# Kernel tuning notes

Measured on AMD Instinct MI355X. Metric: run time of the kernel, lower is better.

The kernel has to match this reference:

```python
import jax, jax.numpy as jnp
import numpy as np

B, T, C, K = 8, 2048, 1024, 128

def setup_inputs() -> dict:
    key = jax.random.key(0)
    k1, k2, k3, k4 = jax.random.split(key, 4)
    scale = 0.02
    return {
        "x": jax.random.normal(k1, (B, T, C), dtype=jnp.float32),
        "Wq": jax.random.normal(k2, (C, K), dtype=jnp.float32) * scale,
        "Wk": jax.random.normal(k3, (C, K), dtype=jnp.float32) * scale,
        "Wv": jax.random.normal(k4, (C, K), dtype=jnp.float32) * scale,
    }

def reference(x, Wq, Wk, Wv):
    # Single-head causal self-attention (ModulUwagi.forward)
    q = jnp.einsum('btc,ck->btk', x, Wq)  # [B,T,K]
    k = jnp.einsum('btc,ck->btk', x, Wk)
    v = jnp.einsum('btc,ck->btk', x, Wv)
    hd = q.shape[-1]
    wei = jnp.einsum('btk,bsk->bts', q, k) * (hd ** -0.5)  # [B,T,T]
    causal = jnp.tril(jnp.ones((x.shape[1], x.shape[1]), dtype=bool))
    wei = jnp.where(causal, wei, -jnp.inf)
    wei = jax.nn.softmax(wei, axis=-1)
    out = jnp.einsum('bts,bsk->btk', wei, v)  # [B,T,K]
    return out
```

## Files before the change

kernel.cpp:

```cpp
#include <hip/hip_runtime.h>
#include <cmath>

#define Bn 8
#define Tn 2048
#define Cn 1024
#define Kn 128

typedef __attribute__((ext_vector_type(8))) short short8;
typedef __attribute__((ext_vector_type(4))) float f32x4;
typedef unsigned short u16;
typedef unsigned int u32;

#define NEGINF (-__builtin_huge_valf())

__device__ __forceinline__ u16 f2b(float f) {
    u32 u = __float_as_uint(f);
    u32 r = (u + 0x7FFFu + ((u >> 16) & 1u)) >> 16;
    return (u16)r;
}
__device__ __forceinline__ float b2f(u16 v) {
    u32 u = ((u32)v) << 16;
    return __uint_as_float(u);
}

__device__ __forceinline__ void load_lds16(const u16* g, u16* l) {
    __builtin_amdgcn_global_load_lds(
        (const __attribute__((address_space(1))) u32*)(g),
        (__attribute__((address_space(3))) u32*)(l), 16, 0, 0);
}

__global__ __launch_bounds__(256)
void prep_kernel(const float* __restrict__ Wq, const float* __restrict__ Wk,
                 const float* __restrict__ Wv, u16* __restrict__ Wt)
{
    int id = blockIdx.x * 256 + threadIdx.x;
    int w   = id >> 15;
    int rem = id & 32767;
    int c   = rem >> 5;
    int n4  = (rem & 31) << 2;
    const float* W = (w == 0) ? Wq : (w == 1) ? Wk : Wv;
    float4 v = *(const float4*)(W + (size_t)c * Kn + n4);
    u16* dst = Wt + (size_t)w * Kn * Cn;
    dst[(size_t)(n4 + 0) * Cn + c] = f2b(v.x);
    dst[(size_t)(n4 + 1) * Cn + c] = f2b(v.y);
    dst[(size_t)(n4 + 2) * Cn + c] = f2b(v.z);
    dst[(size_t)(n4 + 3) * Cn + c] = f2b(v.w);
}

__global__ __launch_bounds__(256)
void proj_kernel(const float* __restrict__ x, const u16* __restrict__ Wt,
                 u16* __restrict__ qkv)
{
    const int bid = blockIdx.x;
    const int g8  = bid >> 3, xr = bid & 7;
    const int w   = g8 % 3;
    const int rt  = (g8 / 3) * 8 + xr;
    const u16* wtg = Wt + (size_t)w * Kn * Cn;
    u16* outp = qkv + (size_t)w * Bn * Tn * Kn;
    const int row0 = rt * 128;
    const int tid  = threadIdx.x;
    const int lane = tid & 63;
    const int wid  = tid >> 6;
    const int l15  = lane & 15, lh = lane >> 4;
    const int wm0 = (wid >> 1) * 64, wn0 = (wid & 1) * 64;

    __shared__ u16 xs[128][72];
    __shared__ u16 wt[128][72];

    f32x4 acc[4][4];
    #pragma unroll
    for (int i = 0; i < 4; ++i)
        #pragma unroll
        for (int j = 0; j < 4; ++j) acc[i][j] = (f32x4){0.f, 0.f, 0.f, 0.f};

    for (int kk = 0; kk < Cn; kk += 64) {
        __syncthreads();
        #pragma unroll
        for (int i = 0; i < 8; ++i) {
            int idx = tid + i * 256;
            int r = idx >> 4, c4 = (idx & 15) << 2;
            float4 xv = *(const float4*)(x + (size_t)(row0 + r) * Cn + kk + c4);
            ushort4 pk = { f2b(xv.x), f2b(xv.y), f2b(xv.z), f2b(xv.w) };
            *(ushort4*)&xs[r][c4] = pk;
        }
        #pragma unroll
        for (int i = 0; i < 4; ++i) {
            int idx = tid + i * 256;
            int n = idx >> 3, c8 = (idx & 7) << 3;
            uint4 wv = *(const uint4*)(wtg + (size_t)n * Cn + kk + c8);
            *(uint4*)&wt[n][c8] = wv;
        }
        __syncthreads();
        #pragma unroll
        for (int kc = 0; kc < 2; ++kc) {
            const int coff = kc * 32 + lh * 8;
            short8 af[4], bf[4];
            #pragma unroll
            for (int mg = 0; mg < 4; ++mg)
                af[mg] = *(const short8*)&xs[wm0 + mg * 16 + l15][coff];
            #pragma unroll
            for (int ng = 0; ng < 4; ++ng)
                bf[ng] = *(const short8*)&wt[wn0 + ng * 16 + l15][coff];
            #pragma unroll
            for (int mg = 0; mg < 4; ++mg)
                #pragma unroll
                for (int ng = 0; ng < 4; ++ng)
                    acc[mg][ng] = __builtin_amdgcn_mfma_f32_16x16x32_bf16(
                        af[mg], bf[ng], acc[mg][ng], 0, 0, 0);
        }
    }
    #pragma unroll
    for (int mg = 0; mg < 4; ++mg)
        #pragma unroll
        for (int ng = 0; ng < 4; ++ng)
            #pragma unroll
            for (int r = 0; r < 4; ++r) {
                int m = row0 + wm0 + mg * 16 + lh * 4 + r;
                int n = wn0 + ng * 16 + l15;
                outp[(size_t)m * Kn + n] = f2b(acc[mg][ng][r]);
            }
}

__device__ const int g_job_qi[32] = {0, 1,1, 2,2,2, 3,3,3,3, 4,4,4,4,
                                     5,5,5,5,5, 6,6,6,6,6,6, 7,7,7,7,7,7,7};
__device__ const int g_sup_b[32] = {0, 0,4, 0,4,8, 0,4,8,12, 0,5,10,15,
                                    0,4,9,14,19, 0,4,9,14,18,23, 0,4,9,13,18,22,27};
__device__ const int g_sup_e[32] = {4, 4,8, 4,8,12, 4,8,12,16, 5,10,15,20,
                                    4,9,14,19,24, 4,9,14,18,23,28, 4,9,13,18,22,27,32};

__global__ __launch_bounds__(512, 2)
void attn_kernel(const u16* __restrict__ qg_, const u16* __restrict__ kg_,
                 const u16* __restrict__ vg_, u16* __restrict__ pO,
                 float* __restrict__ pM, float* __restrict__ pL)
{
    const int b   = blockIdx.x;
    const int job = blockIdx.y;
    const int qi  = g_job_qi[job];
    const int sb  = g_sup_b[job], se = g_sup_e[job];

    const u16* qw = qg_ + (size_t)b * Tn * Kn;
    const u16* kw = kg_ + (size_t)b * Tn * Kn;
    const u16* vw = vg_ + (size_t)b * Tn * Kn;

    const int tid  = threadIdx.x;
    const int lane = tid & 63;
    const int wid  = tid >> 6;
    const int l15  = lane & 15, lh = lane >> 4;

    const int q0 = qi * 256 + wid * 32;
    const int qmax_w = q0 + 31;

    __shared__ u16 lds[32768];

    short8 qf[2][4];
    #pragma unroll
    for (int g = 0; g < 2; ++g)
        #pragma unroll
        for (int kc = 0; kc < 4; ++kc)
            qf[g][kc] = *(const short8*)(qw + (size_t)(q0 + g * 16 + l15) * Kn
                                         + kc * 32 + lh * 8);

    f32x4 acc[8][2];
    #pragma unroll
    for (int dt = 0; dt < 8; ++dt)
        #pragma unroll
        for (int g = 0; g < 2; ++g) acc[dt][g] = (f32x4){0.f, 0.f, 0.f, 0.f};
    float m_g[2] = {NEGINF, NEGINF}, l_g[2] = {0.f, 0.f};

    const float scale = 0.08838834764831843f;

    auto stageK = [&](int sup, int buf) {
        const u16* src = kw + (size_t)sup * 64 * Kn;
        u16* dst = lds + buf * 8192;
        #pragma unroll
        for (int i = 0; i < 2; ++i) {
            int u = wid * 128 + i * 64 + lane;
            int row = u >> 4;
            int c16 = (u & 15) ^ (row & 7);
            load_lds16(src + (size_t)row * Kn + c16 * 8,
                       dst + (size_t)(wid * 128 + i * 64) * 8);
        }
    };
    auto loadV = [&](int sup, uint4* vr) {
        const u16* src = vw + (size_t)sup * 64 * Kn;
        #pragma unroll
        for (int r = 0; r < 2; ++r) {
            int s  = tid & 63;
            int u8 = (tid >> 6) + 8 * r;
            vr[r] = *(const uint4*)(src + (size_t)s * Kn + u8 * 8);
        }
    };
    auto writeV = [&](int buf, const uint4* vr) {
        u16* dst = lds + 16384 + buf * 8192;
        #pragma unroll
        for (int r = 0; r < 2; ++r) {
            int s  = tid & 63;
            int u8 = (tid >> 6) + 8 * r;
            const u16* e = (const u16*)&vr[r];
            #pragma unroll
            for (int j = 0; j < 8; ++j) {
                int d = u8 * 8 + j;
                dst[d * 64 + (((s >> 3) ^ j) << 3) + (s & 7)] = e[j];
            }
        }
    };

    uint4 vreg[2];
    stageK(sb, 0);
    loadV(sb, vreg);
    writeV(0, vreg);

    for (int sup = sb; sup < se; ++sup) {
        const int cur = (sup - sb) & 1;
        __syncthreads();
        const bool have_next = (sup + 1 < se);
        if (have_next) {
            stageK(sup + 1, cur ^ 1);
            loadV(sup + 1, vreg);
        }
        if (sup * 64 <= qmax_w) {
            const u16* Kb = lds + cur * 8192;
            const u16* Vb = lds + 16384 + cur * 8192;
            f32x4 sf[4][2];
            #pragma unroll
            for (int mt = 0; mt < 4; ++mt)
                #pragma unroll
                for (int g = 0; g < 2; ++g) sf[mt][g] = (f32x4){0.f,0.f,0.f,0.f};
            #pragma unroll
            for (int kc = 0; kc < 4; ++kc) {
                short8 a[4];
                #pragma unroll
                for (int mt = 0; mt < 4; ++mt) {
                    int row = mt * 16 + l15;
                    int ch  = (kc * 4 + lh) ^ (row & 7);
                    a[mt] = *(const short8*)(Kb + row * 128 + ch * 8);
                }
                #pragma unroll
                for (int mt = 0; mt < 4; ++mt)
                    #pragma unroll
                    for (int g = 0; g < 2; ++g)
                        sf[mt][g] = __builtin_amdgcn_mfma_f32_16x16x32_bf16(
                            a[mt], qf[g][kc], sf[mt][g], 0, 0, 0);
            }
            const int sbase = sup * 64;
            u32 upk[2][4][2];
            float alpha_g[2];
            #pragma unroll
            for (int g = 0; g < 2; ++g) {
                const int qg = q0 + g * 16 + l15;
                float pv[16];
                float pm = NEGINF;
                #pragma unroll
                for (int mt = 0; mt < 4; ++mt)
                    #pragma unroll
                    for (int r = 0; r < 4; ++r) {
                        int sg = sbase + mt * 16 + lh * 4 + r;
                        float vv = sf[mt][g][r] * scale;
                        vv = (sg > qg) ? NEGINF : vv;
                        pv[mt * 4 + r] = vv;
                        pm = fmaxf(pm, vv);
                    }
                pm = fmaxf(pm, __shfl_xor(pm, 16));
                pm = fmaxf(pm, __shfl_xor(pm, 32));
                float mn  = fmaxf(m_g[g], pm);
                float mns = (mn == NEGINF) ? 0.f : mn;
                float al  = __expf(m_g[g] - mns);
                m_g[g] = mn;
                alpha_g[g] = al;
                float ps = 0.f;
                #pragma unroll
                for (int i = 0; i < 16; ++i) { pv[i] = __expf(pv[i] - mns); ps += pv[i]; }
                ps += __shfl_xor(ps, 16);
                ps += __shfl_xor(ps, 32);
                l_g[g] = l_g[g] * al + ps;
                #pragma unroll
                for (int mt = 0; mt < 4; ++mt)
                    #pragma unroll
                    for (int h = 0; h < 2; ++h)
                        upk[g][mt][h] = (u32)f2b(pv[mt * 4 + 2 * h])
                                      | ((u32)f2b(pv[mt * 4 + 2 * h + 1]) << 16);
            }
            #pragma unroll
            for (int dt = 0; dt < 8; ++dt)
                #pragma unroll
                for (int g = 0; g < 2; ++g)
                    acc[dt][g] *= alpha_g[g];
            #pragma unroll
            for (int ks = 0; ks < 2; ++ks) {
                short8 pf[2];
                #pragma unroll
                for (int g = 0; g < 2; ++g) {
                    union { u32 w[4]; short8 v; } uu;
                    #pragma unroll
                    for (int hp = 0; hp < 4; ++hp) {
                        int srcLane = l15 + 16 * ((lh & 1) * 2 + (hp >> 1));
                        u32 vA = __shfl(upk[g][2 * ks][hp & 1], srcLane, 64);
                        u32 vB = __shfl(upk[g][2 * ks + 1][hp & 1], srcLane, 64);
                        uu.w[hp] = (lh < 2) ? vA : vB;
                    }
                    pf[g] = uu.v;
                }
                #pragma unroll
                for (int dt = 0; dt < 8; ++dt) {
                    int d  = dt * 16 + l15;
                    int ch = (ks * 4 + lh) ^ (d & 7);
                    short8 av = *(const short8*)(Vb + d * 64 + ch * 8);
                    #pragma unroll
                    for (int g = 0; g < 2; ++g)
                        acc[dt][g] = __builtin_amdgcn_mfma_f32_16x16x32_bf16(
                            av, pf[g], acc[dt][g], 0, 0, 0);
                }
            }
        }
        if (have_next) writeV(cur ^ 1, vreg);
    }

    const size_t slotrow = ((size_t)b * 32 + job) * 256 + wid * 32;
    #pragma unroll
    for (int g = 0; g < 2; ++g) {
        size_t row = slotrow + g * 16 + l15;
        #pragma unroll
        for (int dt = 0; dt < 8; ++dt) {
            ushort4 o = { f2b(acc[dt][g][0]), f2b(acc[dt][g][1]),
                          f2b(acc[dt][g][2]), f2b(acc[dt][g][3]) };
            *(ushort4*)(pO + row * 128 + dt * 16 + lh * 4) = o;
        }
        if (lh == 0) {
            pM[row] = m_g[g];
            pL[row] = l_g[g];
        }
    }
}

__device__ const int g_cnt[8] = {1, 2, 3, 4, 4, 5, 6, 7};
__device__ const int g_s0[8]  = {0, 1, 3, 6, 10, 14, 19, 25};

__global__ __launch_bounds__(256)
void merge_kernel(const u16* __restrict__ pO, const float* __restrict__ pM,
                  const float* __restrict__ pL, float* __restrict__ out)
{
    const int bid = blockIdx.x;
    const int b   = bid >> 8;
    const int rem = bid & 255;
    const int qi  = rem >> 5;
    const int rg  = rem & 31;
    const int c = g_cnt[qi], s0 = g_s0[qi];
    const int tid = threadIdx.x;
    const int r8 = tid >> 5;
    const int dg = tid & 31;

    const int row = rg * 8 + r8;
    const size_t base = ((size_t)b * 32 + s0) * 256 + row;

    float mv[8];
    float M = NEGINF;
    #pragma unroll
    for (int i = 0; i < 8; ++i)
        if (i < c) { mv[i] = pM[base + (size_t)i * 256]; M = fmaxf(M, mv[i]); }
    float L = 0.f, w[8];
    #pragma unroll
    for (int i = 0; i < 8; ++i)
        if (i < c) {
            float e = __expf(mv[i] - M);
            L += pL[base + (size_t)i * 256] * e;
            w[i] = e;
        }
    const float invL = 1.f / L;

    float4 o = {0.f, 0.f, 0.f, 0.f};
    #pragma unroll
    for (int i = 0; i < 8; ++i)
        if (i < c) {
            ushort4 p = *(const ushort4*)(pO + (base + (size_t)i * 256) * 128 + dg * 4);
            float wi = w[i] * invL;
            o.x = fmaf(wi, b2f(p.x), o.x);
            o.y = fmaf(wi, b2f(p.y), o.y);
            o.z = fmaf(wi, b2f(p.z), o.z);
            o.w = fmaf(wi, b2f(p.w), o.w);
        }
    *(float4*)(out + ((size_t)b * Tn + qi * 256 + row) * Kn + dg * 4) = o;
}

extern "C" void kernel_launch(void* const* d_in, const int* in_sizes, int n_in,
                              void* d_out, int out_size, void* d_ws, size_t ws_size,
                              hipStream_t stream)
{
    const float* x  = (const float*)d_in[0];
    const float* Wq = (const float*)d_in[1];
    const float* Wk = (const float*)d_in[2];
    const float* Wv = (const float*)d_in[3];
    float* out = (float*)d_out;

    u16* ws = (u16*)d_ws;
    const size_t btk = (size_t)Bn * Tn * Kn;
    u16* q  = ws;
    u16* k  = ws + btk;
    u16* v  = ws + 2 * btk;
    u16* Wt = ws + 3 * btk;
    u16* pO = ws + 3 * btk + 393216;
    float* pM = (float*)(pO + (size_t)8388608);
    float* pL = pM + 65536;

    prep_kernel<<<384, 256, 0, stream>>>(Wq, Wk, Wv, Wt);
    proj_kernel<<<384, 256, 0, stream>>>(x, Wt, ws);
    attn_kernel<<<dim3(Bn, 32), 512, 0, stream>>>(q, k, v, pO, pM, pL);
    merge_kernel<<<2048, 256, 0, stream>>>(pO, pM, pL, out);
}
```

Before: 75.43 us.

## Pre-convert x to bf16 and use a double-buffered async-LDS projection kernel

Adds a combined kernel that transposes the weights and converts x from fp32 to bf16 into workspace. A new projection kernel then streams bf16 x and weight tiles into swizzled, double-buffered LDS with direct-to-LDS loads, using 64-row tiles so the grid has more blocks. The intent is to halve the bytes the GEMM reads for x and to overlap global loads with MFMA work. The cost is an extra pass that writes and rereads a 32 MB bf16 copy of x, plus a fallback path kept for when the workspace is too small.

```diff
diff --git a/kernel.cpp b/kernel.cpp
--- a/kernel.cpp
+++ b/kernel.cpp
@@ -48,6 +48,46 @@
 }
 
 __global__ __launch_bounds__(256)
+void xw_kernel(const float* __restrict__ x,
+               const float* __restrict__ Wq, const float* __restrict__ Wk,
+               const float* __restrict__ Wv, u16* __restrict__ Wt,
+               u16* __restrict__ xbo)
+{
+    const int bid = blockIdx.x;
+    const int tid = threadIdx.x;
+    if (bid < 384) {
+        int id = bid * 256 + tid;
+        int w   = id >> 15;
+        int rem = id & 32767;
+        int c   = rem >> 5;
+        int n4  = (rem & 31) << 2;
+        const float* W = (w == 0) ? Wq : (w == 1) ? Wk : Wv;
+        float4 v = *(const float4*)(W + (size_t)c * Kn + n4);
+        u16* dst = Wt + (size_t)w * Kn * Cn;
+        dst[(size_t)(n4 + 0) * Cn + c] = f2b(v.x);
+        dst[(size_t)(n4 + 1) * Cn + c] = f2b(v.y);
+        dst[(size_t)(n4 + 2) * Cn + c] = f2b(v.z);
+        dst[(size_t)(n4 + 3) * Cn + c] = f2b(v.w);
+    } else {
+        const int id = bid - 384;
+        const float* src = x + (size_t)id * 8192;
+        u16* dst = xbo + (size_t)id * 8192;
+        #pragma unroll
+        for (int it = 0; it < 4; ++it) {
+            const float* s = src + it * 2048 + tid * 8;
+            float4 a = *(const float4*)(s);
+            float4 b = *(const float4*)(s + 4);
+            u32 p0 = (u32)f2b(a.x) | ((u32)f2b(a.y) << 16);
+            u32 p1 = (u32)f2b(a.z) | ((u32)f2b(a.w) << 16);
+            u32 p2 = (u32)f2b(b.x) | ((u32)f2b(b.y) << 16);
+            u32 p3 = (u32)f2b(b.z) | ((u32)f2b(b.w) << 16);
+            uint4 pk = {p0, p1, p2, p3};
+            *(uint4*)(dst + it * 2048 + tid * 8) = pk;
+        }
+    }
+}
+
+__global__ __launch_bounds__(256)
 void proj_kernel(const float* __restrict__ x, const u16* __restrict__ Wt,
                  u16* __restrict__ qkv)
 {
@@ -117,6 +157,89 @@
             for (int r = 0; r < 4; ++r) {
                 int m = row0 + wm0 + mg * 16 + lh * 4 + r;
                 int n = wn0 + ng * 16 + l15;
+                outp[(size_t)m * Kn + n] = f2b(acc[mg][ng][r]);
+            }
+}
+
+__global__ __launch_bounds__(256)
+void proj2_kernel(const u16* __restrict__ xb, const u16* __restrict__ Wt,
+                  u16* __restrict__ qkv)
+{
+    const int bid = blockIdx.x;
+    const int w   = bid % 3;
+    const int rt  = bid / 3;
+    const u16* wtg = Wt + (size_t)w * Kn * Cn;
+    u16* outp = qkv + (size_t)w * Bn * Tn * Kn;
+    const int row0 = rt * 64;
+    const int tid  = threadIdx.x;
+    const int lane = tid & 63;
+    const int wid  = tid >> 6;
+    const int l15  = lane & 15, lh = lane >> 4;
+    const int m0 = (wid >> 1) * 32, n0 = (wid & 1) * 64;
+
+    __shared__ u16 lds[24576];
+
+    auto stage = [&](int kk, int buf) {
+        #pragma unroll
+        for (int i = 0; i < 2; ++i) {
+            int u = tid + i * 256;
+            int row = u >> 3, c8 = u & 7;
+            load_lds16(xb + (size_t)(row0 + row) * Cn + kk + ((c8 ^ (row & 7)) << 3),
+                       lds + buf * 4096 + u * 8);
+        }
+        #pragma unroll
+        for (int i = 0; i < 4; ++i) {
+            int u = tid + i * 256;
+            int n = u >> 3, c8 = u & 7;
+            load_lds16(wtg + (size_t)n * Cn + kk + ((c8 ^ (n & 7)) << 3),
+                       lds + 8192 + buf * 8192 + u * 8);
+        }
+    };
+
+    f32x4 acc[2][4];
+    #pragma unroll
+    for (int i = 0; i < 2; ++i)
+        #pragma unroll
+        for (int j = 0; j < 4; ++j) acc[i][j] = (f32x4){0.f, 0.f, 0.f, 0.f};
+
+    stage(0, 0);
+    for (int step = 0; step < 16; ++step) {
+        const int buf = step & 1;
+        __syncthreads();
+        if (step < 15) stage((step + 1) * 64, buf ^ 1);
+        const u16* Xb = lds + buf * 4096;
+        const u16* Wb = lds + 8192 + buf * 8192;
+        #pragma unroll
+        for (int kc = 0; kc < 2; ++kc) {
+            short8 af[2], bf[4];
+            #pragma unroll
+            for (int mg = 0; mg < 2; ++mg) {
+                int row = m0 + mg * 16 + l15;
+                int ch  = (kc * 4 + lh) ^ (row & 7);
+                af[mg] = *(const short8*)(Xb + row * 64 + ch * 8);
+            }
+            #pragma unroll
+            for (int ng = 0; ng < 4; ++ng) {
+                int n  = n0 + ng * 16 + l15;
+                int ch = (kc * 4 + lh) ^ (n & 7);
+                bf[ng] = *(const short8*)(Wb + n * 64 + ch * 8);
+            }
+            #pragma unroll
+            for (int mg = 0; mg < 2; ++mg)
+                #pragma unroll
+                for (int ng = 0; ng < 4; ++ng)
+                    acc[mg][ng] = __builtin_amdgcn_mfma_f32_16x16x32_bf16(
+                        af[mg], bf[ng], acc[mg][ng], 0, 0, 0);
+        }
+    }
+    #pragma unroll
+    for (int mg = 0; mg < 2; ++mg)
+        #pragma unroll
+        for (int ng = 0; ng < 4; ++ng)
+            #pragma unroll
+            for (int r = 0; r < 4; ++r) {
+                int m = row0 + m0 + mg * 16 + lh * 4 + r;
+                int n = n0 + ng * 16 + l15;
                 outp[(size_t)m * Kn + n] = f2b(acc[mg][ng][r]);
             }
 }
@@ -397,12 +520,26 @@
     u16* k  = ws + btk;
     u16* v  = ws + 2 * btk;
     u16* Wt = ws + 3 * btk;
-    u16* pO = ws + 3 * btk + 393216;
-    float* pM = (float*)(pO + (size_t)8388608);
-    float* pL = pM + 65536;
-
-    prep_kernel<<<384, 256, 0, stream>>>(Wq, Wk, Wv, Wt);
-    proj_kernel<<<384, 256, 0, stream>>>(x, Wt, ws);
-    attn_kernel<<<dim3(Bn, 32), 512, 0, stream>>>(q, k, v, pO, pM, pL);
-    merge_kernel<<<2048, 256, 0, stream>>>(pO, pM, pL, out);
-}
+
+    const size_t X0   = 3 * btk + 393216;
+    const size_t NEED = (X0 + (size_t)16777216) * 2;
+
+    if (ws_size >= NEED) {
+        u16* xb = ws + X0;
+        u16* pO = ws + X0;
+        float* pM = (float*)(pO + (size_t)8388608);
+        float* pL = pM + 65536;
+        xw_kernel<<<2432, 256, 0, stream>>>(x, Wq, Wk, Wv, Wt, xb);
+        proj2_kernel<<<768, 256, 0, stream>>>(xb, Wt, ws);
+        attn_kernel<<<dim3(Bn, 32), 512, 0, stream>>>(q, k, v, pO, pM, pL);
+        merge_kernel<<<2048, 256, 0, stream>>>(pO, pM, pL, out);
+    } else {
+        u16* pO = ws + X0;
+        float* pM = (float*)(pO + (size_t)8388608);
+        float* pL = pM + 65536;
+        prep_kernel<<<384, 256, 0, stream>>>(Wq, Wk, Wv, Wt);
+        proj_kernel<<<384, 256, 0, stream>>>(x, Wt, ws);
+        attn_kernel<<<dim3(Bn, 32), 512, 0, stream>>>(q, k, v, pO, pM, pL);
+        merge_kernel<<<2048, 256, 0, stream>>>(pO, pM, pL, out);
+    }
+}
```

Result: no change. 76.12 us (+0.9%).

## Double-buffer projection GEMM with async W loads, swizzled LDS and packed bf16 convert

Applied to the files above, without the earlier changes.

Rewrites the QKV projection kernel to double-buffer its LDS tiles. The next x tile is prefetched into registers and the next W tile is copied straight into LDS with global_load_lds while MFMAs run on the current buffer, which removes one barrier per step and overlaps memory with compute. The padded LDS arrays are replaced by an XOR-swizzled layout to avoid bank conflicts, and x is converted with v_cvt_pk_bf16_f32 instead of manual rounding. It costs more registers and more LDS per block, which may reduce occupancy.

```diff
diff --git a/kernel.cpp b/kernel.cpp
--- a/kernel.cpp
+++ b/kernel.cpp
@@ -21,6 +21,11 @@
 __device__ __forceinline__ float b2f(u16 v) {
     u32 u = ((u32)v) << 16;
     return __uint_as_float(u);
+}
+__device__ __forceinline__ u32 cvtpk(float lo, float hi) {
+    u32 r;
+    asm("v_cvt_pk_bf16_f32 %0, %1, %2" : "=v"(r) : "v"(lo), "v"(hi));
+    return r;
 }
 
 __device__ __forceinline__ void load_lds16(const u16* g, u16* l) {
@@ -48,8 +53,8 @@
 }
 
 __global__ __launch_bounds__(256)
-void proj_kernel(const float* __restrict__ x, const u16* __restrict__ Wt,
-                 u16* __restrict__ qkv)
+void proj3_kernel(const float* __restrict__ x, const u16* __restrict__ Wt,
+                  u16* __restrict__ qkv)
 {
     const int bid = blockIdx.x;
     const int g8  = bid >> 3, xr = bid & 7;
@@ -62,10 +67,43 @@
     const int lane = tid & 63;
     const int wid  = tid >> 6;
     const int l15  = lane & 15, lh = lane >> 4;
-    const int wm0 = (wid >> 1) * 64, wn0 = (wid & 1) * 64;
-
-    __shared__ u16 xs[128][72];
-    __shared__ u16 wt[128][72];
+    const int m0 = (wid >> 1) * 64, n0 = (wid & 1) * 64;
+
+    __shared__ u16 lds[32768];
+
+    auto stageW = [&](int kk, int buf) {
+        #pragma unroll
+        for (int i = 0; i < 4; ++i) {
+            int u = tid + i * 256;
+            int n = u >> 3, c8 = u & 7;
+            load_lds16(wtg + (size_t)n * Cn + kk + ((c8 ^ (n & 7)) << 3),
+                       lds + 16384 + buf * 8192 + u * 8);
+        }
+    };
+    auto loadX = [&](int kk, float4* xr4) {
+        #pragma unroll
+        for (int i = 0; i < 4; ++i) {
+            int u = tid + i * 256;
+            int r = u >> 3, c8 = u & 7;
+            const float* s = x + (size_t)(row0 + r) * Cn + kk + c8 * 8;
+            xr4[2 * i]     = *(const float4*)(s);
+            xr4[2 * i + 1] = *(const float4*)(s + 4);
+        }
+    };
+    auto writeX = [&](int buf, const float4* xr4) {
+        u16* dst = lds + buf * 8192;
+        #pragma unroll
+        for (int i = 0; i < 4; ++i) {
+            int u = tid + i * 256;
+            int r = u >> 3, c8 = u & 7;
+            uint4 pk;
+            pk.x = cvtpk(xr4[2 * i].x,     xr4[2 * i].y);
+            pk.y = cvtpk(xr4[2 * i].z,     xr4[2 * i].w);
+            pk.z = cvtpk(xr4[2 * i + 1].x, xr4[2 * i + 1].y);
+            pk.w = cvtpk(xr4[2 * i + 1].z, xr4[2 * i + 1].w);
+            *(uint4*)(dst + r * 64 + ((c8 ^ (r & 7)) << 3)) = pk;
+        }
+    };
 
     f32x4 acc[4][4];
     #pragma unroll
@@ -73,34 +111,37 @@
         #pragma unroll
         for (int j = 0; j < 4; ++j) acc[i][j] = (f32x4){0.f, 0.f, 0.f, 0.f};
 
-    for (int kk = 0; kk < Cn; kk += 64) {
+    float4 xcur[8];
+    loadX(0, xcur);
+    stageW(0, 0);
+    writeX(0, xcur);
+
+    for (int step = 0; step < 16; ++step) {
+        const int buf = step & 1;
         __syncthreads();
-        #pragma unroll
-        for (int i = 0; i < 8; ++i) {
-            int idx = tid + i * 256;
-            int r = idx >> 4, c4 = (idx & 15) << 2;
-            float4 xv = *(const float4*)(x + (size_t)(row0 + r) * Cn + kk + c4);
-            ushort4 pk = { f2b(xv.x), f2b(xv.y), f2b(xv.z), f2b(xv.w) };
-            *(ushort4*)&xs[r][c4] = pk;
-        }
-        #pragma unroll
-        for (int i = 0; i < 4; ++i) {
-            int idx = tid + i * 256;
-            int n = idx >> 3, c8 = (idx & 7) << 3;
-            uint4 wv = *(const uint4*)(wtg + (size_t)n * Cn + kk + c8);
-            *(uint4*)&wt[n][c8] = wv;
-        }
-        __syncthreads();
+        const bool nxt = (step < 15);
+        float4 xnext[8];
+        if (nxt) {
+            loadX((step + 1) * 64, xnext);
+            stageW((step + 1) * 64, buf ^ 1);
+        }
+        const u16* Xb = lds + buf * 8192;
+        const u16* Wb = lds + 16384 + buf * 8192;
         #pragma unroll
         for (int kc = 0; kc < 2; ++kc) {
-            const int coff = kc * 32 + lh * 8;
             short8 af[4], bf[4];
             #pragma unroll
-            for (int mg = 0; mg < 4; ++mg)
-                af[mg] = *(const short8*)&xs[wm0 + mg * 16 + l15][coff];
-            #pragma unroll
-            for (int ng = 0; ng < 4; ++ng)
-                bf[ng] = *(const short8*)&wt[wn0 + ng * 16 + l15][coff];
+            for (int mg = 0; mg < 4; ++mg) {
+                int row = m0 + mg * 16 + l15;
+                int ch  = (kc * 4 + lh) ^ (row & 7);
+                af[mg] = *(const short8*)(Xb + row * 64 + ch * 8);
+            }
+            #pragma unroll
+            for (int ng = 0; ng < 4; ++ng) {
+                int n  = n0 + ng * 16 + l15;
+                int ch = (kc * 4 + lh) ^ (n & 7);
+                bf[ng] = *(const short8*)(Wb + n * 64 + ch * 8);
+            }
             #pragma unroll
             for (int mg = 0; mg < 4; ++mg)
                 #pragma unroll
@@ -108,15 +149,17 @@
                     acc[mg][ng] = __builtin_amdgcn_mfma_f32_16x16x32_bf16(
                         af[mg], bf[ng], acc[mg][ng], 0, 0, 0);
         }
+        if (nxt) writeX(buf ^ 1, xnext);
     }
+
     #pragma unroll
     for (int mg = 0; mg < 4; ++mg)
         #pragma unroll
         for (int ng = 0; ng < 4; ++ng)
             #pragma unroll
             for (int r = 0; r < 4; ++r) {
-                int m = row0 + wm0 + mg * 16 + lh * 4 + r;
-                int n = wn0 + ng * 16 + l15;
+                int m = row0 + m0 + mg * 16 + lh * 4 + r;
+                int n = n0 + ng * 16 + l15;
                 outp[(size_t)m * Kn + n] = f2b(acc[mg][ng][r]);
             }
 }
@@ -402,7 +445,7 @@
     float* pL = pM + 65536;
 
     prep_kernel<<<384, 256, 0, stream>>>(Wq, Wk, Wv, Wt);
-    proj_kernel<<<384, 256, 0, stream>>>(x, Wt, ws);
+    proj3_kernel<<<384, 256, 0, stream>>>(x, Wt, ws);
     attn_kernel<<<dim3(Bn, 32), 512, 0, stream>>>(q, k, v, pO, pM, pL);
     merge_kernel<<<2048, 256, 0, stream>>>(pO, pM, pL, out);
 }
```

New measurement: 71.80 us. 4.8% less time.
